# Optimization experiments

Measured on AMD Instinct MI355X. Metric: run time of the kernel, lower is better.

The kernel has to match this reference:

```python
import jax, jax.numpy as jnp
import numpy as np

D_MODEL = 768
NHEAD = 12
HEAD_DIM = D_MODEL // NHEAD
B, L = 8, 1024


def setup_inputs() -> dict:
    key = jax.random.key(0)
    ks = jax.random.split(key, 10)
    s = 0.02  # init scale for weights
    return {
        "x": jax.random.normal(ks[0], (B, L, D_MODEL), dtype=jnp.float32),
        "pos": jax.random.normal(ks[1], (B, L, D_MODEL), dtype=jnp.float32),
        "qkv_w": jax.random.normal(ks[2], (3 * D_MODEL, D_MODEL), dtype=jnp.float32) * s,
        "qkv_b": jnp.zeros((3 * D_MODEL,), dtype=jnp.float32),
        "pq_w": jax.random.normal(ks[3], (D_MODEL, D_MODEL), dtype=jnp.float32) * s,
        "pq_b": jnp.zeros((D_MODEL,), dtype=jnp.float32),
        "pk_w": jax.random.normal(ks[4], (D_MODEL, D_MODEL), dtype=jnp.float32) * s,
        "pk_b": jnp.zeros((D_MODEL,), dtype=jnp.float32),
    }


def reference(x, pos, qkv_w, qkv_b, pq_w, pq_b, pk_w, pk_b):
    b, l, d = x.shape
    h, hd = NHEAD, HEAD_DIM

    qkv = x @ qkv_w.T + qkv_b  # (b, l, 3d)
    q, k, v = jnp.split(qkv, 3, axis=-1)
    # rearrange 'b l (h d) -> b l h d'
    q = q.reshape(b, l, h, hd)
    k = k.reshape(b, l, h, hd)
    v = v.reshape(b, l, h, hd)

    pq = (pos @ pq_w.T + pq_b).reshape(b, l, h, hd)
    pk = (pos @ pk_w.T + pk_b).reshape(b, l, h, hd)

    CC = jnp.einsum('bnhd,blhd->bhnl', q, k)
    CP = jnp.einsum('bnhd,blhd->bhnl', q, pq)
    PC = jnp.einsum('bnhd,blhd->bhnl', k, pk)

    # Faithful to source: only PC is scaled (operator precedence in original)
    scale = (3 * d) ** 0.5
    attn = jax.nn.softmax(CC + CP + PC / scale, axis=-1)

    out = jnp.einsum('bhnl,blhd->bnhd', attn, v)  # (b, n, h, hd)
    return out
```

## Files before the change

### kernel.cpp

```cpp
#include <hip/hip_runtime.h>

#define NHEAD 12
#define BATCH 8
#define SEQ 1024
#define LOG2E 1.4426950408889634f

typedef __bf16 bf16x8 __attribute__((ext_vector_type(8)));
typedef float  f32x4  __attribute__((ext_vector_type(4)));

#define WAITVM0 asm volatile("s_waitcnt vmcnt(0)" ::: "memory")

__device__ __forceinline__ unsigned short f2bf(float f) {
    union { float f; unsigned u; } v; v.f = f;
    unsigned u = v.u;
    u += 0x7fff + ((u >> 16) & 1);
    return (unsigned short)(u >> 16);
}

__device__ __forceinline__ void gload_lds16(const void* g, void* l) {
    __builtin_amdgcn_global_load_lds(
        (const __attribute__((address_space(1))) unsigned*)g,
        (__attribute__((address_space(3))) unsigned*)l, 16, 0, 0);
}

#define SZ_X    6291456
#define SZ_QKVW 1769472
#define SZ_PW   589824
#define CONV_TOTAL 15532032

__global__ __launch_bounds__(256) void convert_kernel(
    const float* __restrict__ x, const float* __restrict__ pos,
    const float* __restrict__ qkv_w, const float* __restrict__ pq_w,
    const float* __restrict__ pk_w, unsigned short* __restrict__ dst)
{
    const size_t i4 = ((size_t)blockIdx.x * 256 + threadIdx.x) * 4;
    if (i4 >= CONV_TOTAL) return;
    const float* src; size_t off;
    if (i4 < SZ_X)                { src = x;     off = i4; }
    else if (i4 < 2 * SZ_X)       { src = pos;   off = i4 - SZ_X; }
    else if (i4 < 2 * SZ_X + SZ_QKVW) { src = qkv_w; off = i4 - 2 * SZ_X; }
    else if (i4 < 2 * SZ_X + SZ_QKVW + SZ_PW) { src = pq_w; off = i4 - 2 * SZ_X - SZ_QKVW; }
    else                          { src = pk_w;  off = i4 - 2 * SZ_X - SZ_QKVW - SZ_PW; }
    float4 v = *(const float4*)(src + off);
    ushort4 o;
    o.x = f2bf(v.x); o.y = f2bf(v.y); o.z = f2bf(v.z); o.w = f2bf(v.w);
    *(ushort4*)(dst + i4) = o;
}


#define PROJ_STAGE(K0, AS, BS) do {                                          \
    const int k0_ = (K0);                                                    \
    const unsigned short* asrc_; int acol_;                                  \
    if (g == 4)                    { asrc_ = posb; acol_ = k0_; }            \
    else if (g == 3 && k0_ >= 768) { asrc_ = posb; acol_ = k0_ - 768; }      \
    else                           { asrc_ = xb;   acol_ = k0_; }            \
    gload_lds16(asrc_ + (size_t)(m0 + r0) * 768 + acol_ + q0 * 8, &AS[base0]);\
    gload_lds16(asrc_ + (size_t)(m0 + r1) * 768 + acol_ + q1 * 8, &AS[base1]);\
    const unsigned short* wsrc_; int wro_, wco_;                             \
    if (g <= 2)       { wsrc_ = qkvw; wro_ = n0;        wco_ = k0_; }        \
    else if (g == 3) {                                                       \
        if (k0_ < 768) { wsrc_ = qkvw; wro_ = n0 - 1536; wco_ = k0_; }       \
        else           { wsrc_ = pqw;  wro_ = n0 - 2304; wco_ = k0_ - 768; } \
    } else            { wsrc_ = pkw;  wro_ = n0 - 3072; wco_ = k0_; }        \
    gload_lds16(wsrc_ + (size_t)(wro_ + r0) * 768 + wco_ + q0 * 8, &BS[base0]);\
    gload_lds16(wsrc_ + (size_t)(wro_ + r1) * 768 + wco_ + q1 * 8, &BS[base1]);\
} while (0)

#define PROJ_COMPUTE(AS, BS) do {                                            \
    bf16x8 af[4], bfr[4];                                                    \
    _Pragma("unroll")                                                        \
    for (int mt = 0; mt < 4; ++mt) {                                         \
        const int rr = wm + mt * 16 + col16;                                 \
        af[mt] = *(const bf16x8*)&AS[rr * 32 + ((quad ^ ((rr >> 1) & 3)) * 8)];\
    }                                                                        \
    _Pragma("unroll")                                                        \
    for (int nt = 0; nt < 4; ++nt) {                                         \
        const int rr = wn + nt * 16 + col16;                                 \
        bfr[nt] = *(const bf16x8*)&BS[rr * 32 + ((quad ^ ((rr >> 1) & 3)) * 8)];\
    }                                                                        \
    _Pragma("unroll")                                                        \
    for (int mt = 0; mt < 4; ++mt)                                           \
        _Pragma("unroll")                                                    \
        for (int nt = 0; nt < 4; ++nt)                                       \
            acc[mt][nt] = __builtin_amdgcn_mfma_f32_16x16x32_bf16(           \
                af[mt], bfr[nt], acc[mt][nt], 0, 0, 0);                      \
} while (0)

__global__ __launch_bounds__(256, 3) void proj_kernel(
    const unsigned short* __restrict__ xb, const unsigned short* __restrict__ posb,
    const unsigned short* __restrict__ qkvw, const unsigned short* __restrict__ pqw,
    const unsigned short* __restrict__ pkw,
    const float* __restrict__ qkv_b, const float* __restrict__ pq_b,
    const float* __restrict__ pk_b,
    unsigned short* __restrict__ Q2, unsigned short* __restrict__ K2,
    unsigned short* __restrict__ Vt, int band)
{
    __shared__ unsigned short As0[128 * 32];
    __shared__ unsigned short As1[128 * 32];
    __shared__ unsigned short Bs0[128 * 32];
    __shared__ unsigned short Bs1[128 * 32];

    const int id  = blockIdx.x;
    const int xcd = id & 7;
    const int idx = id >> 3;
    const int nt30 = (idx / band + 18) % 30;
    const int m0 = (xcd * band + idx % band) * 128;
    const int n0 = nt30 * 128;
    const int g  = n0 / 768;
    const int nk = (g == 3) ? 48 : 24;

    const int tid   = threadIdx.x;
    const int lane  = tid & 63;
    const int w     = tid >> 6;
    const int wm    = (w & 1) * 64;
    const int wn    = (w >> 1) * 64;
    const int quad  = lane >> 4;
    const int col16 = lane & 15;

    const int c0 = w * 64 + lane;
    const int c1 = c0 + 256;
    const int r0 = c0 >> 2, q0 = (c0 & 3) ^ ((c0 >> 3) & 3);
    const int r1 = c1 >> 2, q1 = (c1 & 3) ^ ((c1 >> 3) & 3);
    const int base0 = (w * 64) * 8;
    const int base1 = (w * 64 + 256) * 8;

    f32x4 acc[4][4];
    const f32x4 fzero = {0.f, 0.f, 0.f, 0.f};
#pragma unroll
    for (int mt = 0; mt < 4; ++mt)
#pragma unroll
        for (int nt = 0; nt < 4; ++nt) acc[mt][nt] = fzero;

    PROJ_STAGE(0, As0, Bs0);

    for (int kt = 0; kt < nk; kt += 2) {
        WAITVM0;
        __syncthreads();
        PROJ_STAGE((kt + 1) * 32, As1, Bs1);
        PROJ_COMPUTE(As0, Bs0);

        WAITVM0;
        __syncthreads();
        if (kt + 2 < nk) PROJ_STAGE((kt + 2) * 32, As0, Bs0);
        PROJ_COMPUTE(As1, Bs1);
    }

#pragma unroll
    for (int mt = 0; mt < 4; ++mt) {
        const int mbase = m0 + wm + mt * 16 + quad * 4;
#pragma unroll
        for (int nt = 0; nt < 4; ++nt) {
            const int n = n0 + wn + nt * 16 + col16;
            if (g == 2) {
                const int b = mbase >> 10, l0 = mbase & 1023;
                const int c = n - 1536, h = c >> 6, dd = c & 63;
                ushort4 pk;
                pk.x = f2bf(acc[mt][nt][0] + qkv_b[n]);
                pk.y = f2bf(acc[mt][nt][1] + qkv_b[n]);
                pk.z = f2bf(acc[mt][nt][2] + qkv_b[n]);
                pk.w = f2bf(acc[mt][nt][3] + qkv_b[n]);
                *(ushort4*)&Vt[((size_t)(b * NHEAD + h) * 64 + dd) * 1024 + l0] = pk;
                continue;
            }
#pragma unroll
            for (int r = 0; r < 4; ++r) {
                const int m = mbase + r;
                const int b = m >> 10, l = m & 1023;
                float val = acc[mt][nt][r];
                if (g == 0) {
                    val = (val + qkv_b[n]) * LOG2E;
                    const int h = n >> 6, dd = n & 63;
                    Q2[((size_t)(b * NHEAD + h) * 1024 + l) * 128 + dd] = f2bf(val);
                } else if (g == 1) {
                    val = (val + qkv_b[n]) * (LOG2E / 48.0f);
                    const int c = n - 768, h = c >> 6, dd = c & 63;
                    Q2[((size_t)(b * NHEAD + h) * 1024 + l) * 128 + 64 + dd] = f2bf(val);
                } else if (g == 3) {
                    const int c = n - 2304;
                    val += qkv_b[n - 1536] + pq_b[c];
                    const int h = c >> 6, dd = c & 63;
                    K2[((size_t)(b * NHEAD + h) * 1024 + l) * 128 + dd] = f2bf(val);
                } else {
                    const int c = n - 3072;
                    val += pk_b[c];
                    const int h = c >> 6, dd = c & 63;
                    K2[((size_t)(b * NHEAD + h) * 1024 + l) * 128 + 64 + dd] = f2bf(val);
                }
            }
        }
    }
}


#define ATTN_STAGE(J0, KS, VS) do {                                          \
    const int j0_ = (J0);                                                    \
    gload_lds16(&K2[q2base + (size_t)(j0_ + kr0) * 128 + kc0 * 8], &KS[kbase0]);\
    gload_lds16(&K2[q2base + (size_t)(j0_ + kr1) * 128 + kc1 * 8], &KS[kbase1]);\
    gload_lds16(&Vt[vtbase + (size_t)vr * 1024 + j0_ + vc * 8],    &VS[vbase]);\
} while (0)

#define ATTN_COMPUTE(KS, VS) do {                                            \
    f32x4 st[2][2] = {{fzero, fzero}, {fzero, fzero}};                       \
    _Pragma("unroll")                                                        \
    for (int kk = 0; kk < 4; ++kk) {                                         \
        const int rrj0 = col16, rrj1 = 16 + col16;                           \
        bf16x8 kf0 = *(const bf16x8*)&KS[rrj0 * 128 + (((kk * 4 + quad) ^ (rrj0 & 15)) * 8)];\
        bf16x8 kf1 = *(const bf16x8*)&KS[rrj1 * 128 + (((kk * 4 + quad) ^ (rrj1 & 15)) * 8)];\
        _Pragma("unroll")                                                    \
        for (int qt = 0; qt < 2; ++qt) {                                     \
            st[0][qt] = __builtin_amdgcn_mfma_f32_16x16x32_bf16(kf0, bq[qt][kk], st[0][qt], 0, 0, 0);\
            st[1][qt] = __builtin_amdgcn_mfma_f32_16x16x32_bf16(kf1, bq[qt][kk], st[1][qt], 0, 0, 0);\
        }                                                                    \
    }                                                                        \
    _Pragma("unroll")                                                        \
    for (int qt = 0; qt < 2; ++qt) {                                         \
        float p0[4], p1[4], s = 0.f;                                         \
        _Pragma("unroll")                                                    \
        for (int r = 0; r < 4; ++r) {                                        \
            p0[r] = __builtin_amdgcn_exp2f(st[0][qt][r]);                    \
            p1[r] = __builtin_amdgcn_exp2f(st[1][qt][r]);                    \
            s += p0[r] + p1[r];                                              \
        }                                                                    \
        lsum[qt] += s;                                                       \
        ushort4 pk0, pk1;                                                    \
        pk0.x = f2bf(p0[0]); pk0.y = f2bf(p0[1]); pk0.z = f2bf(p0[2]); pk0.w = f2bf(p0[3]);\
        pk1.x = f2bf(p1[0]); pk1.y = f2bf(p1[1]); pk1.z = f2bf(p1[2]); pk1.w = f2bf(p1[3]);\
        *(ushort4*)&Ps[w][qt * 16 + col16][quad * 4]      = pk0;             \
        *(ushort4*)&Ps[w][qt * 16 + col16][16 + quad * 4] = pk1;             \
    }                                                                        \
    bf16x8 bp[2];                                                            \
    bp[0] = *(const bf16x8*)&Ps[w][col16][quad * 8];                         \
    bp[1] = *(const bf16x8*)&Ps[w][16 + col16][quad * 8];                    \
    _Pragma("unroll")                                                        \
    for (int c2 = 0; c2 < 4; ++c2) {                                         \
        const int rv = c2 * 16 + col16;                                      \
        bf16x8 av = *(const bf16x8*)&VS[rv * 32 + ((quad ^ ((rv >> 2) & 3)) * 8)];\
        _Pragma("unroll")                                                    \
        for (int qt = 0; qt < 2; ++qt)                                       \
            o[qt][c2] = __builtin_amdgcn_mfma_f32_16x16x32_bf16(av, bp[qt], o[qt][c2], 0, 0, 0);\
    }                                                                        \
} while (0)

__global__ __launch_bounds__(256, 4) void attn_kernel(
    const unsigned short* __restrict__ Q2, const unsigned short* __restrict__ K2,
    const unsigned short* __restrict__ Vt, float* __restrict__ out, int b0)
{
    __shared__ unsigned short K2sA[32 * 128];
    __shared__ unsigned short K2sB[32 * 128];
    __shared__ unsigned short VtsA[64 * 32];
    __shared__ unsigned short VtsB[64 * 32];
    __shared__ unsigned short Ps[4][32][40];

    const int bh_l = blockIdx.x;
    const int b = b0 + bh_l / NHEAD, h = bh_l % NHEAD;
    const int tid   = threadIdx.x;
    const int lane  = tid & 63;
    const int w     = tid >> 6;
    const int quad  = lane >> 4;
    const int col16 = lane & 15;
    const int qbase = blockIdx.y * 128 + w * 32;

    const size_t q2base = (size_t)bh_l * 1024 * 128;
    const size_t vtbase = (size_t)bh_l * 64 * 1024;

    const int kL0 = w * 64 + lane, kL1 = kL0 + 256;
    const int kr0 = kL0 >> 4, kc0 = (kL0 & 15) ^ (kr0 & 15);
    const int kr1 = kL1 >> 4, kc1 = (kL1 & 15) ^ (kr1 & 15);
    const int vL  = w * 64 + lane;
    const int vr  = vL >> 2,  vc  = (vL & 3) ^ ((vL >> 4) & 3);
    const int kbase0 = (w * 64) * 8, kbase1 = (w * 64 + 256) * 8;
    const int vbase  = (w * 64) * 8;

    bf16x8 bq[2][4];
#pragma unroll
    for (int qt = 0; qt < 2; ++qt)
#pragma unroll
        for (int kk = 0; kk < 4; ++kk)
            bq[qt][kk] = *(const bf16x8*)&Q2[q2base +
                (size_t)(qbase + qt * 16 + col16) * 128 + kk * 32 + quad * 8];

    f32x4 o[2][4];
    const f32x4 fzero = {0.f, 0.f, 0.f, 0.f};
#pragma unroll
    for (int qt = 0; qt < 2; ++qt)
#pragma unroll
        for (int c2 = 0; c2 < 4; ++c2) o[qt][c2] = fzero;
    float lsum[2] = {0.f, 0.f};

    ATTN_STAGE(0, K2sA, VtsA);

    for (int it = 0; it < SEQ / 32; it += 2) {
        WAITVM0;
        __syncthreads();
        ATTN_STAGE((it + 1) * 32, K2sB, VtsB);
        ATTN_COMPUTE(K2sA, VtsA);

        WAITVM0;
        __syncthreads();
        if (it + 2 < SEQ / 32) ATTN_STAGE((it + 2) * 32, K2sA, VtsA);
        ATTN_COMPUTE(K2sB, VtsB);
    }

#pragma unroll
    for (int qt = 0; qt < 2; ++qt) {
        lsum[qt] += __shfl_xor(lsum[qt], 16, 64);
        lsum[qt] += __shfl_xor(lsum[qt], 32, 64);
    }

#pragma unroll
    for (int qt = 0; qt < 2; ++qt) {
        const float inv = 1.0f / lsum[qt];
        const int q = qbase + qt * 16 + col16;
#pragma unroll
        for (int c2 = 0; c2 < 4; ++c2) {
#pragma unroll
            for (int r = 0; r < 4; ++r) {
                const int dd = c2 * 16 + quad * 4 + r;
                out[(((size_t)(b * 1024 + q)) * 12 + h) * 64 + dd] = o[qt][c2][r] * inv;
            }
        }
    }
}

extern "C" void kernel_launch(void* const* d_in, const int* in_sizes, int n_in,
                              void* d_out, int out_size, void* d_ws, size_t ws_size,
                              hipStream_t stream) {
    const float* x     = (const float*)d_in[0];
    const float* pos   = (const float*)d_in[1];
    const float* qkv_w = (const float*)d_in[2];
    const float* qkv_b = (const float*)d_in[3];
    const float* pq_w  = (const float*)d_in[4];
    const float* pq_b  = (const float*)d_in[5];
    const float* pk_w  = (const float*)d_in[6];
    const float* pk_b  = (const float*)d_in[7];
    float* out = (float*)d_out;

    unsigned short* ws   = (unsigned short*)d_ws;
    unsigned short* xb   = ws;
    unsigned short* posb = xb + SZ_X;
    unsigned short* qkvw = posb + SZ_X;
    unsigned short* pqw  = qkvw + SZ_QKVW;
    unsigned short* pkw  = pqw + SZ_PW;
    unsigned short* cbuf = pkw + SZ_PW;

    const size_t conv_bytes = (size_t)CONV_TOTAL * 2;
    const size_t per_batch  = (size_t)NHEAD * 1024 * 128 * 4
                            + (size_t)NHEAD * 64 * 1024 * 2;
    int cb = BATCH;
    while (cb > 1 && conv_bytes + (size_t)cb * per_batch > ws_size) cb >>= 1;

    unsigned short* Q2 = cbuf;
    unsigned short* K2 = Q2 + (size_t)cb * NHEAD * 1024 * 128;
    unsigned short* Vt = K2 + (size_t)cb * NHEAD * 1024 * 128;

    convert_kernel<<<(CONV_TOTAL / 4 + 255) / 256, 256, 0, stream>>>(
        x, pos, qkv_w, pq_w, pk_w, ws);

    for (int b0 = 0; b0 < BATCH; b0 += cb) {
        proj_kernel<<<dim3(cb * 240), 256, 0, stream>>>(
            xb + (size_t)b0 * 1024 * 768, posb + (size_t)b0 * 1024 * 768,
            qkvw, pqw, pkw, qkv_b, pq_b, pk_b, Q2, K2, Vt, cb);
        attn_kernel<<<dim3(cb * NHEAD, 8), 256, 0, stream>>>(Q2, K2, Vt, out, b0);
    }
}
```

Measured before the change: 248.3 us.

## Software-pipeline attention so PV of the previous tile overlaps QK of the current

Restructures the attention loop so that each phase does the P·V product for the previous key tile and then QK plus softmax for the current one. This uses double-buffered P tiles and triple-buffered V tiles, which lets the P store-to-load dependency and the MFMA chains interleave across tiles. It also replaces manual bf16 rounding with packed float2-to-bfloat162 conversion and lowers the attention occupancy hint from 4 to 3 blocks per CU to fit the extra shared memory. The trade-off is more LDS and registers per block, and fewer resident waves to hide latency.

```diff
diff --git a/kernel.cpp b/kernel.cpp
--- a/kernel.cpp
+++ b/kernel.cpp
@@ -1,4 +1,5 @@
 #include <hip/hip_runtime.h>
+#include <hip/hip_bf16.h>
 
 #define NHEAD 12
 #define BATCH 8
@@ -9,12 +10,20 @@
 typedef float  f32x4  __attribute__((ext_vector_type(4)));
 
 #define WAITVM0 asm volatile("s_waitcnt vmcnt(0)" ::: "memory")
+
+#define MFMA(A, B, C) __builtin_amdgcn_mfma_f32_16x16x32_bf16(A, B, C, 0, 0, 0)
 
 __device__ __forceinline__ unsigned short f2bf(float f) {
     union { float f; unsigned u; } v; v.f = f;
     unsigned u = v.u;
     u += 0x7fff + ((u >> 16) & 1);
     return (unsigned short)(u >> 16);
+}
+
+__device__ __forceinline__ unsigned pkbf(float a, float b) {
+    union { __hip_bfloat162 h; unsigned u; } cv;
+    cv.h = __float22bfloat162_rn(make_float2(a, b));
+    return cv.u;
 }
 
 __device__ __forceinline__ void gload_lds16(const void* g, void* l) {
@@ -82,8 +91,7 @@
     for (int mt = 0; mt < 4; ++mt)                                           \
         _Pragma("unroll")                                                    \
         for (int nt = 0; nt < 4; ++nt)                                       \
-            acc[mt][nt] = __builtin_amdgcn_mfma_f32_16x16x32_bf16(           \
-                af[mt], bfr[nt], acc[mt][nt], 0, 0, 0);                      \
+            acc[mt][nt] = MFMA(af[mt], bfr[nt], acc[mt][nt]);                \
 } while (0)
 
 __global__ __launch_bounds__(256, 3) void proj_kernel(
@@ -154,12 +162,11 @@
             if (g == 2) {
                 const int b = mbase >> 10, l0 = mbase & 1023;
                 const int c = n - 1536, h = c >> 6, dd = c & 63;
-                ushort4 pk;
-                pk.x = f2bf(acc[mt][nt][0] + qkv_b[n]);
-                pk.y = f2bf(acc[mt][nt][1] + qkv_b[n]);
-                pk.z = f2bf(acc[mt][nt][2] + qkv_b[n]);
-                pk.w = f2bf(acc[mt][nt][3] + qkv_b[n]);
-                *(ushort4*)&Vt[((size_t)(b * NHEAD + h) * 64 + dd) * 1024 + l0] = pk;
+                const float bias = qkv_b[n];
+                uint2 pk;
+                pk.x = pkbf(acc[mt][nt][0] + bias, acc[mt][nt][1] + bias);
+                pk.y = pkbf(acc[mt][nt][2] + bias, acc[mt][nt][3] + bias);
+                *(uint2*)&Vt[((size_t)(b * NHEAD + h) * 64 + dd) * 1024 + l0] = pk;
                 continue;
             }
 #pragma unroll
@@ -192,14 +199,26 @@
 }
 
 
-#define ATTN_STAGE(J0, KS, VS) do {                                          \
+#define ATTN_STG(J0, KS, VS) do {                                            \
     const int j0_ = (J0);                                                    \
     gload_lds16(&K2[q2base + (size_t)(j0_ + kr0) * 128 + kc0 * 8], &KS[kbase0]);\
     gload_lds16(&K2[q2base + (size_t)(j0_ + kr1) * 128 + kc1 * 8], &KS[kbase1]);\
     gload_lds16(&Vt[vtbase + (size_t)vr * 1024 + j0_ + vc * 8],    &VS[vbase]);\
 } while (0)
 
-#define ATTN_COMPUTE(KS, VS) do {                                            \
+#define ATTN_PV(VS, PSR) do {                                                \
+    bf16x8 bp0 = *(const bf16x8*)&PSR[w][col16][quad * 8];                   \
+    bf16x8 bp1 = *(const bf16x8*)&PSR[w][16 + col16][quad * 8];              \
+    _Pragma("unroll")                                                        \
+    for (int c2 = 0; c2 < 4; ++c2) {                                         \
+        const int rv = c2 * 16 + col16;                                      \
+        bf16x8 av = *(const bf16x8*)&VS[rv * 32 + ((quad ^ ((rv >> 2) & 3)) * 8)];\
+        o[0][c2] = MFMA(av, bp0, o[0][c2]);                                  \
+        o[1][c2] = MFMA(av, bp1, o[1][c2]);                                  \
+    }                                                                        \
+} while (0)
+
+#define ATTN_QK(KS, PSW) do {                                                \
     f32x4 st[2][2] = {{fzero, fzero}, {fzero, fzero}};                       \
     _Pragma("unroll")                                                        \
     for (int kk = 0; kk < 4; ++kk) {                                         \
@@ -208,8 +227,8 @@
         bf16x8 kf1 = *(const bf16x8*)&KS[rrj1 * 128 + (((kk * 4 + quad) ^ (rrj1 & 15)) * 8)];\
         _Pragma("unroll")                                                    \
         for (int qt = 0; qt < 2; ++qt) {                                     \
-            st[0][qt] = __builtin_amdgcn_mfma_f32_16x16x32_bf16(kf0, bq[qt][kk], st[0][qt], 0, 0, 0);\
-            st[1][qt] = __builtin_amdgcn_mfma_f32_16x16x32_bf16(kf1, bq[qt][kk], st[1][qt], 0, 0, 0);\
+            st[0][qt] = MFMA(kf0, bq[qt][kk], st[0][qt]);                    \
+            st[1][qt] = MFMA(kf1, bq[qt][kk], st[1][qt]);                    \
         }                                                                    \
     }                                                                        \
     _Pragma("unroll")                                                        \
@@ -222,34 +241,33 @@
             s += p0[r] + p1[r];                                              \
         }                                                                    \
         lsum[qt] += s;                                                       \
-        ushort4 pk0, pk1;                                                    \
-        pk0.x = f2bf(p0[0]); pk0.y = f2bf(p0[1]); pk0.z = f2bf(p0[2]); pk0.w = f2bf(p0[3]);\
-        pk1.x = f2bf(p1[0]); pk1.y = f2bf(p1[1]); pk1.z = f2bf(p1[2]); pk1.w = f2bf(p1[3]);\
-        *(ushort4*)&Ps[w][qt * 16 + col16][quad * 4]      = pk0;             \
-        *(ushort4*)&Ps[w][qt * 16 + col16][16 + quad * 4] = pk1;             \
-    }                                                                        \
-    bf16x8 bp[2];                                                            \
-    bp[0] = *(const bf16x8*)&Ps[w][col16][quad * 8];                         \
-    bp[1] = *(const bf16x8*)&Ps[w][16 + col16][quad * 8];                    \
-    _Pragma("unroll")                                                        \
-    for (int c2 = 0; c2 < 4; ++c2) {                                         \
-        const int rv = c2 * 16 + col16;                                      \
-        bf16x8 av = *(const bf16x8*)&VS[rv * 32 + ((quad ^ ((rv >> 2) & 3)) * 8)];\
-        _Pragma("unroll")                                                    \
-        for (int qt = 0; qt < 2; ++qt)                                       \
-            o[qt][c2] = __builtin_amdgcn_mfma_f32_16x16x32_bf16(av, bp[qt], o[qt][c2], 0, 0, 0);\
-    }                                                                        \
-} while (0)
-
-__global__ __launch_bounds__(256, 4) void attn_kernel(
+        uint2 w0, w1;                                                        \
+        w0.x = pkbf(p0[0], p0[1]); w0.y = pkbf(p0[2], p0[3]);                \
+        w1.x = pkbf(p1[0], p1[1]); w1.y = pkbf(p1[2], p1[3]);                \
+        *(uint2*)&PSW[w][qt * 16 + col16][quad * 4]      = w0;               \
+        *(uint2*)&PSW[w][qt * 16 + col16][16 + quad * 4] = w1;               \
+    }                                                                        \
+} while (0)
+
+#define ATTN_PHASE(J, KQK, KST, VPV, VST, PSW, PSR, DOPV, DOST) do {         \
+    WAITVM0;                                                                 \
+    __syncthreads();                                                         \
+    if (DOST) ATTN_STG(((J) + 1) * 32, KST, VST);                            \
+    if (DOPV) ATTN_PV(VPV, PSR);                                             \
+    ATTN_QK(KQK, PSW);                                                       \
+} while (0)
+
+__global__ __launch_bounds__(256, 3) void attn_kernel(
     const unsigned short* __restrict__ Q2, const unsigned short* __restrict__ K2,
     const unsigned short* __restrict__ Vt, float* __restrict__ out, int b0)
 {
     __shared__ unsigned short K2sA[32 * 128];
     __shared__ unsigned short K2sB[32 * 128];
-    __shared__ unsigned short VtsA[64 * 32];
-    __shared__ unsigned short VtsB[64 * 32];
-    __shared__ unsigned short Ps[4][32][40];
+    __shared__ unsigned short VtX[64 * 32];
+    __shared__ unsigned short VtY[64 * 32];
+    __shared__ unsigned short VtZ[64 * 32];
+    __shared__ unsigned short Ps0[4][32][40];
+    __shared__ unsigned short Ps1[4][32][40];
 
     const int bh_l = blockIdx.x;
     const int b = b0 + bh_l / NHEAD, h = bh_l % NHEAD;
@@ -287,19 +305,22 @@
         for (int c2 = 0; c2 < 4; ++c2) o[qt][c2] = fzero;
     float lsum[2] = {0.f, 0.f};
 
-    ATTN_STAGE(0, K2sA, VtsA);
-
-    for (int it = 0; it < SEQ / 32; it += 2) {
-        WAITVM0;
-        __syncthreads();
-        ATTN_STAGE((it + 1) * 32, K2sB, VtsB);
-        ATTN_COMPUTE(K2sA, VtsA);
-
-        WAITVM0;
-        __syncthreads();
-        if (it + 2 < SEQ / 32) ATTN_STAGE((it + 2) * 32, K2sA, VtsA);
-        ATTN_COMPUTE(K2sB, VtsB);
-    }
+    ATTN_STG(0, K2sA, VtX);
+
+    ATTN_PHASE(0, K2sA, K2sB, VtZ, VtY, Ps0, Ps1, 0, 1);
+
+    for (int j = 1; j < 31; j += 6) {
+        ATTN_PHASE(j + 0, K2sB, K2sA, VtX, VtZ, Ps1, Ps0, 1, 1);
+        ATTN_PHASE(j + 1, K2sA, K2sB, VtY, VtX, Ps0, Ps1, 1, 1);
+        ATTN_PHASE(j + 2, K2sB, K2sA, VtZ, VtY, Ps1, Ps0, 1, 1);
+        ATTN_PHASE(j + 3, K2sA, K2sB, VtX, VtZ, Ps0, Ps1, 1, 1);
+        ATTN_PHASE(j + 4, K2sB, K2sA, VtY, VtX, Ps1, Ps0, 1, 1);
+        ATTN_PHASE(j + 5, K2sA, K2sB, VtZ, VtY, Ps0, Ps1, 1, 1);
+    }
+
+    ATTN_PHASE(31, K2sB, K2sA, VtX, VtZ, Ps1, Ps0, 1, 0);
+
+    ATTN_PV(VtY, Ps1);
 
 #pragma unroll
     for (int qt = 0; qt < 2; ++qt) {
```

Result: no change. 243.6 us (-1.9%).
